# Performance work log

Measured on AMD Instinct MI355X. Metric: run time of the kernel, lower is better.

## Reference

```python
import jax, jax.numpy as jnp
import numpy as np

INPUT_DIM = 1024
HIDDEN_DIM = 1024 * 16
K = 32
BATCH = 4096


def setup_inputs() -> dict:
    key = jax.random.key(0)
    k1, k2, k3 = jax.random.split(key, 3)
    x = jax.random.normal(k1, (BATCH, INPUT_DIM), dtype=jnp.float32)
    # kaiming_normal_ init: std = sqrt(2 / fan_in); torch Linear weight is [out, in]
    W_enc = jax.random.normal(k2, (HIDDEN_DIM, INPUT_DIM), dtype=jnp.float32) * np.sqrt(2.0 / INPUT_DIM)
    b_enc = jnp.zeros((HIDDEN_DIM,), dtype=jnp.float32)
    W_dec = jax.random.normal(k3, (INPUT_DIM, HIDDEN_DIM), dtype=jnp.float32) * np.sqrt(2.0 / HIDDEN_DIM)
    b_dec = jnp.zeros((INPUT_DIM,), dtype=jnp.float32)
    return {"x": x, "W_enc": W_enc, "b_enc": b_enc, "W_dec": W_dec, "b_dec": b_dec}


def _top_k_activation(enc, k):
    # topk of |enc| per row, scatter a 0/1 mask, multiply (matches torch code)
    _, idx = jax.lax.top_k(jnp.abs(enc), k)          # [B, k]
    rows = jnp.arange(enc.shape[0])[:, None]          # [B, 1]
    mask = jnp.zeros_like(enc).at[rows, idx].set(1.0)
    return enc * mask


def reference(x, W_enc, b_enc, W_dec, b_dec):
    encoded = x @ W_enc.T + b_enc                     # [B, H]
    sparse_encoded = _top_k_activation(encoded, K)    # [B, H], k nonzeros/row
    decoded = sparse_encoded @ W_dec.T + b_dec        # [B, D]
    return (sparse_encoded, decoded)
```

## Files before the change

### kernel.cpp

```cpp
#include <hip/hip_runtime.h>
#include <cstdint>
#include <cstddef>

#define BATCH   4096
#define IN_DIM  1024
#define HID     16384
#define KSEL    32

#define BKK 32

typedef float f32x4_t __attribute__((ext_vector_type(4)));

__global__ __launch_bounds__(512, 8)
void enc_gemm(const float* __restrict__ X, const float* __restrict__ W,
              const float* __restrict__ bias, float* __restrict__ C)
{
    __shared__ __align__(16) float Bs[128 * BKK];

    const int bn = blockIdx.x;
    const int bm = blockIdx.y;
    const int t  = threadIdx.x;
    const int lane = t & 63;
    const int wid  = t >> 6;

    float acc[8][2];
#pragma unroll
    for (int r = 0; r < 8; ++r) { acc[r][0] = 0.f; acc[r][1] = 0.f; }

    const float* Wb = W + (size_t)(bn * 128) * IN_DIM;

    const unsigned rowByte = (unsigned)__builtin_amdgcn_readfirstlane(
        (int)((unsigned)(bm * 64 + wid * 8) * (unsigned)(IN_DIM * 4)));
    const char* aBase = (const char*)X + rowByte;

    const int bswz = lane & 7;
    const float* bRow0 = Bs + (size_t)lane * BKK;
    const float* bRow1 = Bs + (size_t)(lane + 64) * BKK;

    for (int k0 = 0; k0 < IN_DIM; k0 += BKK) {
#pragma unroll
        for (int q = 0; q < 2; ++q) {
            const int s  = q * 512 + t;
            const int m  = s >> 3;
            const int gc = (s & 7) ^ (m & 7);
            __builtin_amdgcn_global_load_lds(
                (const __attribute__((address_space(1))) void*)(Wb + (size_t)m * IN_DIM + k0 + gc * 4),
                (__attribute__((address_space(3))) void*)(Bs + s * 4), 16, 0, 0);
        }
        __syncthreads();

#pragma unroll
        for (int kq = 0; kq < 8; ++kq) {
            const float4 b0 = *(const float4*)(bRow0 + ((kq ^ bswz) * 4));
            const float4 b1 = *(const float4*)(bRow1 + ((kq ^ bswz) * 4));

            const char* apq = aBase + (size_t)(k0 + kq * 4) * 4;
            f32x4_t a0, a1, a2, a3, a4, a5, a6, a7;
            asm volatile(
                "s_load_dwordx4 %[r0], %[ap], 0x0\n\t"
                "s_load_dwordx4 %[r1], %[ap], 0x1000\n\t"
                "s_load_dwordx4 %[r2], %[ap], 0x2000\n\t"
                "s_load_dwordx4 %[r3], %[ap], 0x3000\n\t"
                "s_load_dwordx4 %[r4], %[ap], 0x4000\n\t"
                "s_load_dwordx4 %[r5], %[ap], 0x5000\n\t"
                "s_load_dwordx4 %[r6], %[ap], 0x6000\n\t"
                "s_load_dwordx4 %[r7], %[ap], 0x7000\n\t"
                "s_waitcnt lgkmcnt(0)"
                : [r0]"=s"(a0), [r1]"=s"(a1), [r2]"=s"(a2), [r3]"=s"(a3),
                  [r4]"=s"(a4), [r5]"=s"(a5), [r6]"=s"(a6), [r7]"=s"(a7)
                : [ap]"s"(apq));

#define ROW_FMA(AV, R)                                   \
            acc[R][0] = fmaf(AV.x, b0.x, acc[R][0]);     \
            acc[R][1] = fmaf(AV.x, b1.x, acc[R][1]);     \
            acc[R][0] = fmaf(AV.y, b0.y, acc[R][0]);     \
            acc[R][1] = fmaf(AV.y, b1.y, acc[R][1]);     \
            acc[R][0] = fmaf(AV.z, b0.z, acc[R][0]);     \
            acc[R][1] = fmaf(AV.z, b1.z, acc[R][1]);     \
            acc[R][0] = fmaf(AV.w, b0.w, acc[R][0]);     \
            acc[R][1] = fmaf(AV.w, b1.w, acc[R][1]);
            ROW_FMA(a0, 0) ROW_FMA(a1, 1) ROW_FMA(a2, 2) ROW_FMA(a3, 3)
            ROW_FMA(a4, 4) ROW_FMA(a5, 5) ROW_FMA(a6, 6) ROW_FMA(a7, 7)
#undef ROW_FMA
        }
        __syncthreads();
    }

    const int r0 = bm * 64 + wid * 8;
    const int c0 = bn * 128 + lane;
    const float bv0 = bias[c0];
    const float bv1 = bias[c0 + 64];
#pragma unroll
    for (int r = 0; r < 8; ++r) {
        C[(size_t)(r0 + r) * HID + c0]      = acc[r][0] + bv0;
        C[(size_t)(r0 + r) * HID + c0 + 64] = acc[r][1] + bv1;
    }
}

__global__ __launch_bounds__(256)
void topk_rows(float* __restrict__ E, int* __restrict__ idx_out,
               float* __restrict__ val_out)
{
    const int row = blockIdx.x;
    float* p = E + (size_t)row * HID;
    const int t    = threadIdx.x;
    const int lane = t & 63;
    const int wid  = t >> 6;

    __shared__ __align__(16) float row_s[HID];
    __shared__ unsigned h8[8][257];
    __shared__ unsigned hist[256];
    __shared__ unsigned wsum[4];
    __shared__ unsigned s_prefix;
    __shared__ int s_rank, s_eq, s_cnt;

#pragma unroll
    for (int c = 0; c < 16; ++c) {
        const int s = c * 256 + t;
        __builtin_amdgcn_global_load_lds(
            (const __attribute__((address_space(1))) void*)(p + (size_t)s * 4),
            (__attribute__((address_space(3))) void*)(row_s + s * 4), 16, 0, 0);
    }
    for (int i = t; i < 8 * 257; i += 256) ((unsigned*)h8)[i] = 0u;
    if (t == 0) { s_rank = KSEL; s_prefix = 0u; s_eq = 0; s_cnt = 0; }
    __syncthreads();

    unsigned* myh = h8[t & 7];
#pragma unroll
    for (int c = 0; c < 16; ++c) {
        const float4 v = *(const float4*)(row_s + (c * 256 + t) * 4);
        const float vv[4] = {v.x, v.y, v.z, v.w};
#pragma unroll
        for (int j = 0; j < 4; ++j)
            atomicAdd(&myh[(__float_as_uint(vv[j]) & 0x7FFFFFFFu) >> 23], 1u);
    }
    __syncthreads();

    const int psh_arr[4]  = {31, 23, 15, 7};
    const int sh_arr[4]   = {23, 15, 7, 0};
    const unsigned msk[4] = {255u, 255u, 255u, 127u};
    const int bits_arr[4] = {8, 8, 8, 7};

#pragma unroll
    for (int lvl = 0; lvl < 4; ++lvl) {
        const int r = s_rank;
        const unsigned pfx = s_prefix;

        unsigned mycnt;
        if (lvl == 0) {
            unsigned m = 0;
#pragma unroll
            for (int c = 0; c < 8; ++c) m += h8[c][t];
            mycnt = m;
        } else {
            hist[t] = 0u;
            __syncthreads();
            const int psh = psh_arr[lvl];
            const int sh  = sh_arr[lvl];
#pragma unroll
            for (int c = 0; c < 16; ++c) {
                const float4 v = *(const float4*)(row_s + (c * 256 + t) * 4);
                const float vv[4] = {v.x, v.y, v.z, v.w};
#pragma unroll
                for (int j = 0; j < 4; ++j) {
                    const unsigned k = __float_as_uint(vv[j]) & 0x7FFFFFFFu;
                    if ((k >> psh) == pfx)
                        atomicAdd(&hist[(k >> sh) & msk[lvl]], 1u);
                }
            }
            __syncthreads();
            mycnt = hist[t];
        }

        unsigned sv = mycnt;
#pragma unroll
        for (int off = 1; off < 64; off <<= 1) {
            const unsigned u = __shfl_down(sv, off, 64);
            sv += (lane + off < 64) ? u : 0u;
        }
        if (lane == 0) wsum[wid] = sv;
        __syncthreads();
        unsigned above = 0;
        for (int ww = wid + 1; ww < 4; ++ww) above += wsum[ww];
        const unsigned suff  = sv + above;
        const unsigned suffn = suff - mycnt;
        if (suff >= (unsigned)r && suffn < (unsigned)r) {
            s_rank   = r - (int)suffn;
            s_prefix = (pfx << bits_arr[lvl]) | (unsigned)t;
        }
        __syncthreads();
    }

    const unsigned vkey = s_prefix;
    const int eq_need   = s_rank;

#pragma unroll
    for (int c = 0; c < 16; ++c) {
        const int i0 = (c * 256 + t) * 4;
        const float4 v = *(const float4*)(row_s + i0);
        float vv[4] = {v.x, v.y, v.z, v.w};
#pragma unroll
        for (int j = 0; j < 4; ++j) {
            const unsigned k = __float_as_uint(vv[j]) & 0x7FFFFFFFu;
            bool keep = false;
            if (k > vkey) keep = true;
            else if (k == vkey) {
                const int slot = atomicAdd(&s_eq, 1);
                if (slot < eq_need) keep = true;
            }
            if (keep) {
                const int ls = atomicAdd(&s_cnt, 1);
                idx_out[row * KSEL + ls] = i0 + j;
                val_out[row * KSEL + ls] = vv[j];
            } else {
                vv[j] = 0.f;
            }
        }
        float4 o; o.x = vv[0]; o.y = vv[1]; o.z = vv[2]; o.w = vv[3];
        *(float4*)(p + i0) = o;
    }
}

__global__ __launch_bounds__(256)
void transpose_wdec(const float* __restrict__ Wd, float* __restrict__ WdT)
{
    __shared__ float tile[32][33];
    const int bx = blockIdx.x;
    const int by = blockIdx.y;
    const int t  = threadIdx.x;
    const int lx = t & 31, ly = t >> 5;
#pragma unroll
    for (int r = 0; r < 32; r += 8)
        tile[ly + r][lx] = Wd[(size_t)(by * 32 + ly + r) * HID + bx * 32 + lx];
    __syncthreads();
#pragma unroll
    for (int r = 0; r < 32; r += 8)
        WdT[(size_t)(bx * 32 + ly + r) * IN_DIM + by * 32 + lx] = tile[lx][ly + r];
}

__global__ __launch_bounds__(256)
void decode_rows(const float* __restrict__ WdT, const float* __restrict__ bd,
                 const int* __restrict__ idxs, const float* __restrict__ vals,
                 float* __restrict__ out)
{
    const int row = blockIdx.x;
    const int d   = threadIdx.x * 4;
    float4 acc = *(const float4*)(bd + d);
    for (int i = 0; i < KSEL; ++i) {
        const int   j = idxs[row * KSEL + i];
        const float v = vals[row * KSEL + i];
        const float4 w = *(const float4*)(WdT + (size_t)j * IN_DIM + d);
        acc.x = fmaf(v, w.x, acc.x);
        acc.y = fmaf(v, w.y, acc.y);
        acc.z = fmaf(v, w.z, acc.z);
        acc.w = fmaf(v, w.w, acc.w);
    }
    *(float4*)(out + (size_t)row * IN_DIM + d) = acc;
}

__global__ __launch_bounds__(256)
void decode_rows_noT(const float* __restrict__ Wd, const float* __restrict__ bd,
                     const int* __restrict__ idxs, const float* __restrict__ vals,
                     float* __restrict__ out)
{
    const int row = blockIdx.x;
    const int d0  = threadIdx.x * 4;
    float acc[4];
#pragma unroll
    for (int q = 0; q < 4; ++q) acc[q] = bd[d0 + q];
    for (int i = 0; i < KSEL; ++i) {
        const int   j = idxs[row * KSEL + i];
        const float v = vals[row * KSEL + i];
#pragma unroll
        for (int q = 0; q < 4; ++q)
            acc[q] = fmaf(v, Wd[(size_t)(d0 + q) * HID + j], acc[q]);
    }
#pragma unroll
    for (int q = 0; q < 4; ++q) out[(size_t)row * IN_DIM + d0 + q] = acc[q];
}

extern "C" void kernel_launch(void* const* d_in, const int* in_sizes, int n_in,
                              void* d_out, int out_size, void* d_ws, size_t ws_size,
                              hipStream_t stream)
{
    const float* x     = (const float*)d_in[0];
    const float* W_enc = (const float*)d_in[1];
    const float* b_enc = (const float*)d_in[2];
    const float* W_dec = (const float*)d_in[3];
    const float* b_dec = (const float*)d_in[4];

    float* out     = (float*)d_out;
    float* sparse  = out;
    float* decoded = out + (size_t)BATCH * HID;

    const size_t list_bytes = (size_t)BATCH * KSEL * 4;
    const size_t wdt_bytes  = (size_t)HID * IN_DIM * 4;
    int*   idx_l = (int*)d_ws;
    float* val_l = (float*)((char*)d_ws + list_bytes);
    float* WdT   = (float*)((char*)d_ws + 2 * list_bytes);
    const bool have_wdt = ws_size >= 2 * list_bytes + wdt_bytes;

    enc_gemm<<<dim3(HID / 128, BATCH / 64), 512, 0, stream>>>(x, W_enc, b_enc, sparse);

    topk_rows<<<BATCH, 256, 0, stream>>>(sparse, idx_l, val_l);

    if (have_wdt) {
        transpose_wdec<<<dim3(HID / 32, IN_DIM / 32), 256, 0, stream>>>(W_dec, WdT);
        decode_rows<<<BATCH, 256, 0, stream>>>(WdT, b_dec, idx_l, val_l, decoded);
    } else {
        decode_rows_noT<<<BATCH, 256, 0, stream>>>(W_dec, b_dec, idx_l, val_l, decoded);
    }
}
```

Measured before the change: 2.068 ms.

## Widen encoder GEMM tile to 256 columns and use compiler scalar loads

The encoder GEMM block tile grows from 64x128 to 64x256, so each thread keeps 4 column accumulators per row instead of 2. Each scalar-loaded X value now feeds twice as many FMAs, and the grid shrinks by half. The inline-asm s_load block with its forced waitcnt is replaced by constant-address-space pointer loads, so the compiler can schedule the scalar loads itself. The cost is more registers and twice the shared memory per block, which may reduce occupancy.

```diff
diff --git a/kernel.cpp b/kernel.cpp
--- a/kernel.cpp
+++ b/kernel.cpp
@@ -10,12 +10,13 @@
 #define BKK 32
 
 typedef float f32x4_t __attribute__((ext_vector_type(4)));
+typedef const __attribute__((address_space(4))) f32x4_t* cvec4_t;
 
 __global__ __launch_bounds__(512, 8)
 void enc_gemm(const float* __restrict__ X, const float* __restrict__ W,
               const float* __restrict__ bias, float* __restrict__ C)
 {
-    __shared__ __align__(16) float Bs[128 * BKK];
+    __shared__ __align__(16) float Bs[256 * BKK];
 
     const int bn = blockIdx.x;
     const int bm = blockIdx.y;
@@ -23,23 +24,28 @@
     const int lane = t & 63;
     const int wid  = t >> 6;
 
-    float acc[8][2];
-#pragma unroll
-    for (int r = 0; r < 8; ++r) { acc[r][0] = 0.f; acc[r][1] = 0.f; }
-
-    const float* Wb = W + (size_t)(bn * 128) * IN_DIM;
+    float acc[8][4];
+#pragma unroll
+    for (int r = 0; r < 8; ++r)
+#pragma unroll
+        for (int j = 0; j < 4; ++j) acc[r][j] = 0.f;
+
+    const float* Wb = W + (size_t)(bn * 256) * IN_DIM;
 
     const unsigned rowByte = (unsigned)__builtin_amdgcn_readfirstlane(
         (int)((unsigned)(bm * 64 + wid * 8) * (unsigned)(IN_DIM * 4)));
-    const char* aBase = (const char*)X + rowByte;
+    const __attribute__((address_space(4))) char* aBase =
+        (const __attribute__((address_space(4))) char*)((const char*)X + rowByte);
 
     const int bswz = lane & 7;
     const float* bRow0 = Bs + (size_t)lane * BKK;
     const float* bRow1 = Bs + (size_t)(lane + 64) * BKK;
+    const float* bRow2 = Bs + (size_t)(lane + 128) * BKK;
+    const float* bRow3 = Bs + (size_t)(lane + 192) * BKK;
 
     for (int k0 = 0; k0 < IN_DIM; k0 += BKK) {
 #pragma unroll
-        for (int q = 0; q < 2; ++q) {
+        for (int q = 0; q < 4; ++q) {
             const int s  = q * 512 + t;
             const int m  = s >> 3;
             const int gc = (s & 7) ^ (m & 7);
@@ -53,32 +59,36 @@
         for (int kq = 0; kq < 8; ++kq) {
             const float4 b0 = *(const float4*)(bRow0 + ((kq ^ bswz) * 4));
             const float4 b1 = *(const float4*)(bRow1 + ((kq ^ bswz) * 4));
-
-            const char* apq = aBase + (size_t)(k0 + kq * 4) * 4;
-            f32x4_t a0, a1, a2, a3, a4, a5, a6, a7;
-            asm volatile(
-                "s_load_dwordx4 %[r0], %[ap], 0x0\n\t"
-                "s_load_dwordx4 %[r1], %[ap], 0x1000\n\t"
-                "s_load_dwordx4 %[r2], %[ap], 0x2000\n\t"
-                "s_load_dwordx4 %[r3], %[ap], 0x3000\n\t"
-                "s_load_dwordx4 %[r4], %[ap], 0x4000\n\t"
-                "s_load_dwordx4 %[r5], %[ap], 0x5000\n\t"
-                "s_load_dwordx4 %[r6], %[ap], 0x6000\n\t"
-                "s_load_dwordx4 %[r7], %[ap], 0x7000\n\t"
-                "s_waitcnt lgkmcnt(0)"
-                : [r0]"=s"(a0), [r1]"=s"(a1), [r2]"=s"(a2), [r3]"=s"(a3),
-                  [r4]"=s"(a4), [r5]"=s"(a5), [r6]"=s"(a6), [r7]"=s"(a7)
-                : [ap]"s"(apq));
+            const float4 b2 = *(const float4*)(bRow2 + ((kq ^ bswz) * 4));
+            const float4 b3 = *(const float4*)(bRow3 + ((kq ^ bswz) * 4));
+
+            cvec4_t ap = (cvec4_t)(aBase + (size_t)(k0 + kq * 4) * 4);
+            const f32x4_t a0 = ap[0 * 256];
+            const f32x4_t a1 = ap[1 * 256];
+            const f32x4_t a2 = ap[2 * 256];
+            const f32x4_t a3 = ap[3 * 256];
+            const f32x4_t a4 = ap[4 * 256];
+            const f32x4_t a5 = ap[5 * 256];
+            const f32x4_t a6 = ap[6 * 256];
+            const f32x4_t a7 = ap[7 * 256];
 
 #define ROW_FMA(AV, R)                                   \
             acc[R][0] = fmaf(AV.x, b0.x, acc[R][0]);     \
             acc[R][1] = fmaf(AV.x, b1.x, acc[R][1]);     \
+            acc[R][2] = fmaf(AV.x, b2.x, acc[R][2]);     \
+            acc[R][3] = fmaf(AV.x, b3.x, acc[R][3]);     \
             acc[R][0] = fmaf(AV.y, b0.y, acc[R][0]);     \
             acc[R][1] = fmaf(AV.y, b1.y, acc[R][1]);     \
+            acc[R][2] = fmaf(AV.y, b2.y, acc[R][2]);     \
+            acc[R][3] = fmaf(AV.y, b3.y, acc[R][3]);     \
             acc[R][0] = fmaf(AV.z, b0.z, acc[R][0]);     \
             acc[R][1] = fmaf(AV.z, b1.z, acc[R][1]);     \
+            acc[R][2] = fmaf(AV.z, b2.z, acc[R][2]);     \
+            acc[R][3] = fmaf(AV.z, b3.z, acc[R][3]);     \
             acc[R][0] = fmaf(AV.w, b0.w, acc[R][0]);     \
-            acc[R][1] = fmaf(AV.w, b1.w, acc[R][1]);
+            acc[R][1] = fmaf(AV.w, b1.w, acc[R][1]);     \
+            acc[R][2] = fmaf(AV.w, b2.w, acc[R][2]);     \
+            acc[R][3] = fmaf(AV.w, b3.w, acc[R][3]);
             ROW_FMA(a0, 0) ROW_FMA(a1, 1) ROW_FMA(a2, 2) ROW_FMA(a3, 3)
             ROW_FMA(a4, 4) ROW_FMA(a5, 5) ROW_FMA(a6, 6) ROW_FMA(a7, 7)
 #undef ROW_FMA
@@ -87,13 +97,16 @@
     }
 
     const int r0 = bm * 64 + wid * 8;
-    const int c0 = bn * 128 + lane;
-    const float bv0 = bias[c0];
-    const float bv1 = bias[c0 + 64];
+    const int c0 = bn * 256 + lane;
+    float bv[4];
+#pragma unroll
+    for (int j = 0; j < 4; ++j) bv[j] = bias[c0 + j * 64];
 #pragma unroll
     for (int r = 0; r < 8; ++r) {
-        C[(size_t)(r0 + r) * HID + c0]      = acc[r][0] + bv0;
-        C[(size_t)(r0 + r) * HID + c0 + 64] = acc[r][1] + bv1;
+        const size_t rowoff = (size_t)(r0 + r) * HID + c0;
+#pragma unroll
+        for (int j = 0; j < 4; ++j)
+            C[rowoff + j * 64] = acc[r][j] + bv[j];
     }
 }
 
@@ -300,7 +313,7 @@
     float* WdT   = (float*)((char*)d_ws + 2 * list_bytes);
     const bool have_wdt = ws_size >= 2 * list_bytes + wdt_bytes;
 
-    enc_gemm<<<dim3(HID / 128, BATCH / 64), 512, 0, stream>>>(x, W_enc, b_enc, sparse);
+    enc_gemm<<<dim3(HID / 256, BATCH / 64), 512, 0, stream>>>(x, W_enc, b_enc, sparse);
 
     topk_rows<<<BATCH, 256, 0, stream>>>(sparse, idx_l, val_l);
 
```

Result: slower. 6.093 ms (+194.7%).
